# Performance work log

Measured on AMD Instinct MI355X. Metric: run time of the kernel, lower is better.

Reference implementation:

```python
import jax, jax.numpy as jnp
import numpy as np

NDIM = 256
NKNOT = 32
N = 131072


def setup_inputs() -> dict:
    key = jax.random.key(0)
    k1, k2 = jax.random.split(key)
    x = jax.random.normal(k1, (N, NDIM), dtype=jnp.float32)
    x0 = jax.random.uniform(k2, (NDIM, 1), dtype=jnp.float32) - 4.5
    logdx = jnp.ones((NDIM, NKNOT - 1), jnp.float32) * jnp.log(jnp.abs(-2.0 * x0 / (NKNOT - 1)))
    return {
        "x": x,
        "x0": x0,
        "y0": x0,
        "logdx": logdx,
        "logdy": logdx,
        "logderiv": jnp.zeros((NDIM, NKNOT), jnp.float32),
    }


def _prepare(x0, y0, logdx, logdy, logderiv):
    xx = jnp.concatenate([x0, x0 + jnp.cumsum(jnp.exp(logdx), axis=1)], axis=1)  # (ndim, nknot)
    yy = jnp.concatenate([y0, y0 + jnp.cumsum(jnp.exp(logdy), axis=1)], axis=1)
    delta = jnp.exp(logderiv)
    return xx, yy, delta


def _rqspline_fwd(x, x0, y0, logdx, logdy, logderiv):
    nknot = logderiv.shape[1]
    xx, yy, delta = _prepare(x0, y0, logdx, logdy, logderiv)
    xt = x.T  # (ndim, N)
    # bucket index per dimension; knots are constants for the search (detached in torch)
    idx = jax.vmap(jnp.searchsorted)(jax.lax.stop_gradient(xx), jax.lax.stop_gradient(xt))  # (ndim, N)
    k = jnp.clip(idx, 1, nknot - 1)

    g = lambda a, j: jnp.take_along_axis(a, j, axis=1)
    xk, xkm = g(xx, k), g(xx, k - 1)
    yk, ykm = g(yy, k), g(yy, k - 1)
    dk, dkm = g(delta, k), g(delta, k - 1)

    interior = (idx > 0) & (idx < nknot)
    xi = jnp.where(interior, (xt - xkm) / (xk - xkm), 0.5)  # safe value off-branch
    s = (yk - ykm) / (xk - xkm)
    xi1_xi = xi * (1.0 - xi)
    xi2 = xi * xi
    denom = s + (dk + dkm - 2.0 * s) * xi1_xi
    y_int = ykm + (yk - ykm) * (s * xi2 + dkm * xi1_xi) / denom
    ld_int = (2.0 * jnp.log(s)
              + jnp.log(dk * xi2 + 2.0 * s * xi1_xi + dkm * (1.0 - xi) ** 2)
              - 2.0 * jnp.log(denom))

    # linear extrapolation below first / above last knot
    y_lo = yy[:, :1] + (xt - xx[:, :1]) * delta[:, :1]
    y_hi = yy[:, -1:] + (xt - xx[:, -1:]) * delta[:, -1:]
    ld_lo = jnp.broadcast_to(logderiv[:, :1], xt.shape)
    ld_hi = jnp.broadcast_to(logderiv[:, -1:], xt.shape)

    y = jnp.where(idx == 0, y_lo, jnp.where(idx == nknot, y_hi, y_int))
    ld = jnp.where(idx == 0, ld_lo, jnp.where(idx == nknot, ld_hi, ld_int))
    return y.T, ld.T


def reference(x, x0, y0, logdx, logdy, logderiv):
    return _rqspline_fwd(x, x0, y0, logdx, logdy, logderiv)
```

## Files before the change

### kernel.cpp

```cpp
#include <hip/hip_runtime.h>
#include <hip/hip_bf16.h>

#define NDIM  256
#define NKNOT 32
#define DPB   64
#define BLOCK 256
#define ROWS_PER_ITER (BLOCK / DPB)

__global__ __launch_bounds__(BLOCK) void rqspline_kernel(
    const float* __restrict__ x,
    const float* __restrict__ x0,
    const float* __restrict__ y0,
    const float* __restrict__ logdx,
    const float* __restrict__ logdy,
    const float* __restrict__ logderiv,
    float* __restrict__ y_out,
    float* __restrict__ ld_out,
    int n_rows, int rows_per_tile)
{
    __shared__ float sXX[NKNOT * DPB];
    __shared__ float sYY[NKNOT * DPB];
    __shared__ float sDD[NKNOT * DPB];
    __shared__ float sL0[DPB];
    __shared__ float sL1[DPB];

    const int t  = threadIdx.x;
    const int d0 = blockIdx.y * DPB;

    if (t < DPB) {
        const int d = d0 + t;
        float acc = x0[d];
        sXX[t] = acc;
        #pragma unroll
        for (int j = 1; j < NKNOT; ++j) {
            acc += __expf(logdx[d * (NKNOT - 1) + j - 1]);
            sXX[j * DPB + t] = acc;
        }
    } else if (t < 2 * DPB) {
        const int dl = t - DPB, d = d0 + dl;
        float acc = y0[d];
        sYY[dl] = acc;
        #pragma unroll
        for (int j = 1; j < NKNOT; ++j) {
            acc += __expf(logdy[d * (NKNOT - 1) + j - 1]);
            sYY[j * DPB + dl] = acc;
        }
    } else if (t < 3 * DPB) {
        const int dl = t - 2 * DPB, d = d0 + dl;
        sL0[dl] = logderiv[d * NKNOT];
        sL1[dl] = logderiv[d * NKNOT + NKNOT - 1];
    }
    #pragma unroll
    for (int m = t; m < DPB * NKNOT; m += BLOCK) {
        const int j  = m & (NKNOT - 1);
        const int dl = m >> 5;
        sDD[j * DPB + dl] = __expf(logderiv[(d0 + dl) * NKNOT + j]);
    }
    __syncthreads();

    const int dl = t & (DPB - 1);
    const int rs = t >> 6;
    const int d  = d0 + dl;
    const int row0    = blockIdx.x * rows_per_tile;
    const int row_end = min(row0 + rows_per_tile, n_rows);

    const float ld_lo = sL0[dl];
    const float ld_hi = sL1[dl];

    for (int r = row0 + rs; r < row_end; r += ROWS_PER_ITER) {
        const size_t base = (size_t)r * NDIM + d;
        const float v = x[base];

        int idx = (sXX[15 * DPB + dl] < v) ? 16 : 0;
        idx += (sXX[(idx + 7) * DPB + dl] < v) ? 8 : 0;
        idx += (sXX[(idx + 3) * DPB + dl] < v) ? 4 : 0;
        idx += (sXX[(idx + 1) * DPB + dl] < v) ? 2 : 0;
        idx += (sXX[(idx    ) * DPB + dl] < v) ? 1 : 0;
        idx += (sXX[31 * DPB + dl] < v) ? 1 : 0;

        const int kk = min(max(idx, 1), NKNOT - 1);
        const int ak = kk * DPB + dl;
        const float xk  = sXX[ak], xkm = sXX[ak - DPB];
        const float yk  = sYY[ak], ykm = sYY[ak - DPB];
        const float dk  = sDD[ak], dkm = sDD[ak - DPB];

        const float dx  = xk - xkm;
        const float dy  = yk - ykm;
        const float inv = __builtin_amdgcn_rcpf(dx);
        const float xi  = (v - xkm) * inv;
        const float s   = dy * inv;
        const float omxi = 1.0f - xi;
        const float xi2  = xi * xi;
        const float x1x  = xi * omxi;
        const float denom  = s + (dk + dkm - 2.0f * s) * x1x;
        const float invden = __builtin_amdgcn_rcpf(denom);
        const float y_int  = ykm + dy * (s * xi2 + dkm * x1x) * invden;
        const float aa = dk * xi2 + 2.0f * s * x1x + dkm * omxi * omxi;
        const float ld_int = __logf(s * s * aa * (invden * invden));

        const bool lo = (idx == 0);
        const bool hi = (idx >= NKNOT);
        const float xb = lo ? xkm : xk;
        const float yb = lo ? ykm : yk;
        const float db = lo ? dkm : dk;
        const float y_b  = yb + (v - xb) * db;
        const float ld_b = lo ? ld_lo : ld_hi;
        const bool interior = !(lo || hi);

        y_out[base]  = interior ? y_int  : y_b;
        ld_out[base] = interior ? ld_int : ld_b;
    }
}

extern "C" void kernel_launch(void* const* d_in, const int* in_sizes, int n_in,
                              void* d_out, int out_size, void* d_ws, size_t ws_size,
                              hipStream_t stream) {
    const float* x        = (const float*)d_in[0];
    const float* x0       = (const float*)d_in[1];
    const float* y0       = (const float*)d_in[2];
    const float* logdx    = (const float*)d_in[3];
    const float* logdy    = (const float*)d_in[4];
    const float* logderiv = (const float*)d_in[5];

    const int N = in_sizes[0] / NDIM;
    float* y_out  = (float*)d_out;
    float* ld_out = y_out + (size_t)N * NDIM;

    const int rows_per_tile = 512;
    dim3 grid((N + rows_per_tile - 1) / rows_per_tile, NDIM / DPB);
    rqspline_kernel<<<grid, BLOCK, 0, stream>>>(
        x, x0, y0, logdx, logdy, logderiv, y_out, ld_out, N, rows_per_tile);
}
```

Measured before the change: 442.9 us.

## Unroll row loop by four, interleave searches, and resize grid

The row loop is unrolled four ways so each thread issues four global loads, then runs four interleaved binary searches and gathers over LDS before computing and storing, which exposes more memory and LDS latency hiding. The grid is reshaped to about 384 row tiles with rows per tile rounded to the unroll stride, and launch bounds request six blocks per CU. 32-bit offsets replace size_t indexing. The cost is higher register pressure and fewer, longer-running blocks.

```diff
diff --git a/kernel.cpp b/kernel.cpp
--- a/kernel.cpp
+++ b/kernel.cpp
@@ -5,9 +5,11 @@
 #define NKNOT 32
 #define DPB   64
 #define BLOCK 256
-#define ROWS_PER_ITER (BLOCK / DPB)
-
-__global__ __launch_bounds__(BLOCK) void rqspline_kernel(
+#define RPI   (BLOCK / DPB)
+#define U     4
+#define STRIDE (RPI * U)
+
+__global__ __launch_bounds__(BLOCK, 6) void rqspline_kernel(
     const float* __restrict__ x,
     const float* __restrict__ x0,
     const float* __restrict__ y0,
@@ -66,10 +68,85 @@
 
     const float ld_lo = sL0[dl];
     const float ld_hi = sL1[dl];
-
-    for (int r = row0 + rs; r < row_end; r += ROWS_PER_ITER) {
-        const size_t base = (size_t)r * NDIM + d;
-        const float v = x[base];
+    const float xTop15 = 0.0f;
+
+    int r = row0;
+    for (; r + STRIDE <= row_end; r += STRIDE) {
+        unsigned off[U];
+        float v[U];
+        #pragma unroll
+        for (int u = 0; u < U; ++u) {
+            off[u] = (unsigned)(r + rs + u * RPI) * NDIM + d;
+            v[u] = x[off[u]];
+        }
+
+        const float mid15 = sXX[15 * DPB + dl];
+        const float top31 = sXX[31 * DPB + dl];
+        int idx[U];
+        #pragma unroll
+        for (int u = 0; u < U; ++u) idx[u]  = (mid15 < v[u]) ? 16 : 0;
+        #pragma unroll
+        for (int u = 0; u < U; ++u) idx[u] += (sXX[(idx[u] + 7) * DPB + dl] < v[u]) ? 8 : 0;
+        #pragma unroll
+        for (int u = 0; u < U; ++u) idx[u] += (sXX[(idx[u] + 3) * DPB + dl] < v[u]) ? 4 : 0;
+        #pragma unroll
+        for (int u = 0; u < U; ++u) idx[u] += (sXX[(idx[u] + 1) * DPB + dl] < v[u]) ? 2 : 0;
+        #pragma unroll
+        for (int u = 0; u < U; ++u) idx[u] += (sXX[(idx[u]    ) * DPB + dl] < v[u]) ? 1 : 0;
+        #pragma unroll
+        for (int u = 0; u < U; ++u) idx[u] += (top31 < v[u]) ? 1 : 0;
+
+        float xk[U], xkm[U], yk[U], ykm[U], dk[U], dkm[U];
+        int ak[U];
+        #pragma unroll
+        for (int u = 0; u < U; ++u) {
+            const int kk = min(max(idx[u], 1), NKNOT - 1);
+            ak[u] = kk * DPB + dl;
+        }
+        #pragma unroll
+        for (int u = 0; u < U; ++u) { xk[u] = sXX[ak[u]]; xkm[u] = sXX[ak[u] - DPB]; }
+        #pragma unroll
+        for (int u = 0; u < U; ++u) { yk[u] = sYY[ak[u]]; ykm[u] = sYY[ak[u] - DPB]; }
+        #pragma unroll
+        for (int u = 0; u < U; ++u) { dk[u] = sDD[ak[u]]; dkm[u] = sDD[ak[u] - DPB]; }
+
+        float yv[U], ldv[U];
+        #pragma unroll
+        for (int u = 0; u < U; ++u) {
+            const float dx  = xk[u] - xkm[u];
+            const float dy  = yk[u] - ykm[u];
+            const float inv = __builtin_amdgcn_rcpf(dx);
+            const float xi  = (v[u] - xkm[u]) * inv;
+            const float s   = dy * inv;
+            const float omxi = 1.0f - xi;
+            const float xi2  = xi * xi;
+            const float x1x  = xi * omxi;
+            const float denom  = s + (dk[u] + dkm[u] - 2.0f * s) * x1x;
+            const float invden = __builtin_amdgcn_rcpf(denom);
+            const float y_int  = ykm[u] + dy * (s * xi2 + dkm[u] * x1x) * invden;
+            const float aa = dk[u] * xi2 + 2.0f * s * x1x + dkm[u] * omxi * omxi;
+            const float ld_int = __logf(s * s * aa * (invden * invden));
+
+            const bool lo = (idx[u] == 0);
+            const bool hi = (idx[u] >= NKNOT);
+            const float xb = lo ? xkm[u] : xk[u];
+            const float yb = lo ? ykm[u] : yk[u];
+            const float db = lo ? dkm[u] : dk[u];
+            const float y_b  = yb + (v[u] - xb) * db;
+            const float ld_b = lo ? ld_lo : ld_hi;
+            const bool interior = !(lo || hi);
+            yv[u]  = interior ? y_int  : y_b;
+            ldv[u] = interior ? ld_int : ld_b;
+        }
+        #pragma unroll
+        for (int u = 0; u < U; ++u) y_out[off[u]] = yv[u];
+        #pragma unroll
+        for (int u = 0; u < U; ++u) ld_out[off[u]] = ldv[u];
+    }
+
+    for (int rr = r + rs; rr < row_end; rr += RPI) {
+        const unsigned off1 = (unsigned)rr * NDIM + d;
+        const float v = x[off1];
 
         int idx = (sXX[15 * DPB + dl] < v) ? 16 : 0;
         idx += (sXX[(idx + 7) * DPB + dl] < v) ? 8 : 0;
@@ -107,8 +184,8 @@
         const float ld_b = lo ? ld_lo : ld_hi;
         const bool interior = !(lo || hi);
 
-        y_out[base]  = interior ? y_int  : y_b;
-        ld_out[base] = interior ? ld_int : ld_b;
+        y_out[off1]  = interior ? y_int  : y_b;
+        ld_out[off1] = interior ? ld_int : ld_b;
     }
 }
 
@@ -126,8 +203,11 @@
     float* y_out  = (float*)d_out;
     float* ld_out = y_out + (size_t)N * NDIM;
 
-    const int rows_per_tile = 512;
-    dim3 grid((N + rows_per_tile - 1) / rows_per_tile, NDIM / DPB);
+    int bx  = 384;
+    int rpt = (N + bx - 1) / bx;
+    rpt = (rpt + STRIDE - 1) / STRIDE * STRIDE;
+    bx  = (N + rpt - 1) / rpt;
+    dim3 grid(bx, NDIM / DPB);
     rqspline_kernel<<<grid, BLOCK, 0, stream>>>(
-        x, x0, y0, logdx, logdy, logderiv, y_out, ld_out, N, rows_per_tile);
+        x, x0, y0, logdx, logdy, logderiv, y_out, ld_out, N, rpt);
 }
```

New measurement: 387.0 us. 1.14x faster.
